# Kernel tuning notes

Hardware: AMD Instinct MI355X
Metric: run time of the kernel (lower is better)

Reference implementation:

```python
import jax, jax.numpy as jnp
import numpy as np
import itertools

# 3x3x3 neighborhood geometry: 27 cells, offsets in itertools.product order,
# so index 13 is the center voxel.
_POS = np.array(list(itertools.product([-1, 0, 1], repeat=3)))  # [27,3]
_DIFF = _POS[:, None, :] - _POS[None, :, :]
_A18 = (np.abs(_DIFF).sum(-1) <= 2)   # 18-connectivity (scipy structure s in source)
_A26 = (np.abs(_DIFF).max(-1) <= 1)   # 26-connectivity (np.ones((3,3,3)))
_CENTER = 13


def _cc_label_6(fg):
    """Connected-component labels of 3D bool array under 6-connectivity
    (scipy.ndimage.label default structure). Background = 0; each component
    gets a distinct positive id (min linear index + 1) via min-propagation."""
    n = fg.size
    BIG = jnp.int32(n + 2)
    idx = jnp.arange(1, n + 1, dtype=jnp.int32).reshape(fg.shape)
    lab0 = jnp.where(fg, idx, BIG)

    def step(lab):
        p = jnp.pad(lab, 1, mode='constant', constant_values=n + 2)
        m = lab
        m = jnp.minimum(m, p[:-2, 1:-1, 1:-1])
        m = jnp.minimum(m, p[2:, 1:-1, 1:-1])
        m = jnp.minimum(m, p[1:-1, :-2, 1:-1])
        m = jnp.minimum(m, p[1:-1, 2:, 1:-1])
        m = jnp.minimum(m, p[1:-1, 1:-1, :-2])
        m = jnp.minimum(m, p[1:-1, 1:-1, 2:])
        return jnp.where(fg, m, BIG)

    def cond(c):
        return c[1]

    def body(c):
        lab = c[0]
        new = step(lab)
        return (new, jnp.any(new != lab))

    lab, _ = jax.lax.while_loop(cond, body, (lab0, jnp.array(True)))
    return jnp.where(fg, lab, 0)


def _count_components(mask, adj_np):
    """mask: [V,27] bool. Counts connected components of the True cells in each
    27-cell neighborhood under adjacency adj_np (matches scipy label num_features).
    Min-label propagation for 26 steps (>= max path length in a 27-node graph)."""
    BIG = jnp.int32(27)
    ids = jnp.arange(27, dtype=jnp.int32)
    adj = jnp.asarray(adj_np)
    init = jnp.where(mask, ids[None, :], BIG)

    def body(_, lab):
        new = lab
        for j in range(27):
            contrib = jnp.where(mask[:, j], lab[:, j], BIG)[:, None]  # [V,1]
            new = jnp.minimum(new, jnp.where(adj[:, j][None, :], contrib, BIG))
        return jnp.where(mask, new, BIG)

    lab = jax.lax.fori_loop(0, 26, body, init)
    # a component's root keeps its own index -> count roots
    return jnp.sum(mask & (lab == ids[None, :]), axis=1)  # [V]


def _nonsimple_points(x, threshold=0.5):
    """JAX version of label_nonsimple_points: 1.0 where voxel is a non-simple
    point of the thresholded volume, else 0.0."""
    D, H, W = x.shape
    fg = x > threshold
    lab = _cc_label_6(fg)                       # [D,H,W] int32, 0 = background
    p = jnp.pad(lab, 1, mode='edge')            # np.pad(..., 'edge') in source
    nb = jnp.stack(
        [p[dz + 1:dz + 1 + D, dy + 1:dy + 1 + H, dx + 1:dx + 1 + W]
         for dz, dy, dx in _POS], axis=-1).reshape(-1, 27)  # [V,27]
    center = nb[:, _CENTER]
    # Test 1: cells differing from the center's component id (incl. background),
    # 18-connectivity; simple requires exactly one component.
    c1 = _count_components(nb != center[:, None], _A18)
    # Test 2: cells equal to the center's component, center removed,
    # 26-connectivity; simple requires exactly one component.
    m2 = (nb == center[:, None]).at[:, _CENTER].set(False)
    c2 = _count_components(m2, _A26)
    ns = (center != 0) & ((c1 != 1) | (c2 != 1))
    return ns.reshape(x.shape).astype(x.dtype)


def _weight_tensor(x, simple_weight=1.0, non_simple_weight=10.0):
    ns = jax.lax.stop_gradient(_nonsimple_points(x))
    w = simple_weight * (1.0 - ns) + non_simple_weight * ns
    return w * x


def setup_inputs() -> dict:
    key = jax.random.key(0)
    k1, k2 = jax.random.split(key)
    pred = jax.random.normal(k1, (64, 64, 64), dtype=jnp.float32)
    target = jax.random.uniform(k2, (64, 64, 64), dtype=jnp.float32)
    return {"pred": pred, "target": target}


def reference(pred, target):
    wp = _weight_tensor(pred)
    wl = _weight_tensor(target)
    # err = -(wl * -log(1+e^{-wp}) + (1-wl) * -log(1+e^{wp}))
    err = wl * jax.nn.softplus(-wp) + (1.0 - wl) * jax.nn.softplus(wp)
    return jnp.sum(err)
```

## Files before the change

### kernel.cpp

```cpp
#include <hip/hip_runtime.h>

#define NINV 0xFFFFFFFFu
static constexpr int D = 64, H = 64, W = 64;
static constexpr int NVOX = D * H * W;
static constexpr int NTOT = 2 * NVOX;


__device__ __forceinline__ unsigned find_c(unsigned* P, unsigned i) {
    unsigned p = P[i];
    while (p != i) {
        unsigned gp = P[p];
        if (gp == p) return p;
        P[i] = gp;
        i = gp;
        p = P[i];
    }
    return i;
}

__device__ void unite(unsigned* P, unsigned a, unsigned b) {
    for (;;) {
        a = find_c(P, a);
        b = find_c(P, b);
        if (a == b) return;
        if (a > b) { unsigned t = a; a = b; b = t; }
        unsigned old = atomicCAS(&P[b], b, a);
        if (old == b || old == a) return;
        b = old;
    }
}


__global__ __launch_bounds__(512) void local_ccl_k(const float* __restrict__ pred,
                                                   const float* __restrict__ target,
                                                   unsigned* __restrict__ parent) {
    __shared__ unsigned lab[512];
    int tb  = blockIdx.x & 511;
    int vol = blockIdx.x >> 9;
    const float* src = vol ? target : pred;
    int tx = (tb & 7) << 3;
    int ty = ((tb >> 3) & 7) << 3;
    int tz = (tb >> 6) << 3;

    int l = threadIdx.x;
    int lx = l & 7, ly = (l >> 3) & 7, lz = l >> 6;
    int g = ((tz + lz) << 12) + ((ty + ly) << 6) + (tx + lx);

    bool fg = src[g] > 0.5f;
    lab[l] = fg ? (unsigned)l : NINV;
    __syncthreads();

    for (;;) {
        int my_changed = 0;
        if (fg) {
            unsigned cur = lab[l];
            unsigned m = cur;
            if (lx > 0) m = min(m, lab[l - 1]);
            if (lx < 7) m = min(m, lab[l + 1]);
            if (ly > 0) m = min(m, lab[l - 8]);
            if (ly < 7) m = min(m, lab[l + 8]);
            if (lz > 0) m = min(m, lab[l - 64]);
            if (lz < 7) m = min(m, lab[l + 64]);
            for (;;) { unsigned p = lab[m]; if (p >= m) break; m = p; }
            if (m < cur) { lab[l] = m; my_changed = 1; }
        }
        if (__syncthreads_count(my_changed) == 0) break;
    }

    unsigned r = NINV;
    if (fg) {
        unsigned rr = lab[l];
        r = (unsigned)(vol * NVOX)
          + (unsigned)(((tz + (int)(rr >> 6)) << 12)
                     + ((ty + (int)((rr >> 3) & 7)) << 6)
                     +  (tx + (int)(rr & 7)));
    }
    parent[vol * NVOX + g] = r;
}


static constexpr int FACES_PER_DIR = 7 * 8 * 8;
static constexpr int FACES_PER_VOL = 3 * FACES_PER_DIR;
static constexpr int FACES_TOT     = 2 * FACES_PER_VOL;

__global__ void merge_k(unsigned* __restrict__ parent) {
    int wave = (int)((blockIdx.x * blockDim.x + threadIdx.x) >> 6);
    int lane = threadIdx.x & 63;
    if (wave >= FACES_TOT) return;
    int vol = wave / FACES_PER_VOL;
    int f   = wave - vol * FACES_PER_VOL;
    int dir = f / FACES_PER_DIR;
    int ff  = f - dir * FACES_PER_DIR;
    int plane = ff >> 6;
    int tf    = ff & 63;
    int a0 = ((tf & 7) << 3) + (lane & 7);
    int a1 = ((tf >> 3) << 3) + (lane >> 3);
    int x, y, z, stride;
    if (dir == 0)      { x = plane * 8 + 7; y = a0; z = a1; stride = 1; }
    else if (dir == 1) { y = plane * 8 + 7; x = a0; z = a1; stride = 64; }
    else               { z = plane * 8 + 7; x = a0; y = a1; stride = 4096; }
    int i = vol * NVOX + (z << 12) + (y << 6) + x;

    unsigned ra = parent[i];
    unsigned rb = parent[i + stride];
    bool valid = (ra != NINV) && (rb != NINV);
    unsigned long long key = valid ? (((unsigned long long)ra << 32) | rb) : ~0ull;

    bool leader = valid;
    #pragma unroll 8
    for (int j = 0; j < 64; ++j) {
        unsigned long long kj = __shfl(key, j, 64);
        if (j < lane && kj == key) leader = false;
    }
    if (leader) unite(parent, ra, rb);
}


__global__ void flatten_k(unsigned* __restrict__ parent) {
    int i = blockIdx.x * blockDim.x + threadIdx.x;
    if (i >= NTOT) return;
    unsigned p = parent[i];
    if (p == NINV) return;
    unsigned r = p, q;
    while ((q = parent[r]) != r) r = q;
    parent[i] = r;
}


__device__ __forceinline__ int count_components(unsigned mask, const unsigned* adj) {
    int count = 0;
    while (mask) {
        unsigned comp = mask & (0u - mask);
        for (;;) {
            unsigned acc = comp;
            unsigned t = comp;
            while (t) {
                int b = __ffs(t) - 1;
                acc |= adj[b];
                t &= t - 1;
            }
            acc &= mask;
            if (acc == comp) break;
            comp = acc;
        }
        mask &= ~comp;
        ++count;
    }
    return count;
}

__device__ __forceinline__ float weight_lds(const unsigned* __restrict__ h,
                                            int lx, int ly, int lz,
                                            const unsigned* sA18, const unsigned* sA26) {
    int ctr = (lz + 1) * 100 + (ly + 1) * 10 + (lx + 1);
    unsigned c = h[ctr];
    if (c == NINV) return 1.0f;
    unsigned same = 0;
    int k = 0;
    #pragma unroll
    for (int dz = 0; dz <= 2; ++dz) {
        #pragma unroll
        for (int dy = 0; dy <= 2; ++dy) {
            int base = (lz + dz) * 100 + (ly + dy) * 10 + lx;
            #pragma unroll
            for (int dx = 0; dx <= 2; ++dx) {
                same |= (h[base + dx] == c ? 1u : 0u) << k;
                ++k;
            }
        }
    }
    unsigned mask1 = (~same) & 0x07FFFFFFu;
    unsigned mask2 = same & ~(1u << 13);
    int c1 = count_components(mask1, sA18);
    int c2 = count_components(mask2, sA26);
    return ((c1 != 1) || (c2 != 1)) ? 10.0f : 1.0f;
}

__global__ __launch_bounds__(512) void final_k(const float* __restrict__ pred,
                                               const float* __restrict__ target,
                                               const unsigned* __restrict__ labP,
                                               const unsigned* __restrict__ labT,
                                               float* __restrict__ out) {
    __shared__ unsigned sA18[27], sA26[27];
    __shared__ unsigned hP[1000], hT[1000];
    __shared__ float sred[8];

    int l = threadIdx.x;
    if (l < 27) {
        int iz = l / 9, iy = (l / 3) % 3, ix = l % 3;
        unsigned m18 = 0, m26 = 0;
        for (int j = 0; j < 27; ++j) {
            int jz = j / 9, jy = (j / 3) % 3, jx = j % 3;
            int az = iz - jz; az = az < 0 ? -az : az;
            int ay = iy - jy; ay = ay < 0 ? -ay : ay;
            int ax = ix - jx; ax = ax < 0 ? -ax : ax;
            if (az + ay + ax <= 2) m18 |= 1u << j;
            if (az <= 1 && ay <= 1 && ax <= 1) m26 |= 1u << j;
        }
        sA18[l] = m18; sA26[l] = m26;
    }

    int tb = blockIdx.x;
    int tx = (tb & 7) << 3;
    int ty = ((tb >> 3) & 7) << 3;
    int tz = (tb >> 6) << 3;

    for (int e = l; e < 1000; e += 512) {
        int hx = e % 10, hy = (e / 10) % 10, hz = e / 100;
        int gx = min(max(tx + hx - 1, 0), 63);
        int gy = min(max(ty + hy - 1, 0), 63);
        int gz = min(max(tz + hz - 1, 0), 63);
        int g = (gz << 12) + (gy << 6) + gx;
        hP[e] = labP[g];
        hT[e] = labT[g];
    }
    __syncthreads();

    int lx = l & 7, ly = (l >> 3) & 7, lz = l >> 6;
    int g = ((tz + lz) << 12) + ((ty + ly) << 6) + (tx + lx);

    float wP = weight_lds(hP, lx, ly, lz, sA18, sA26);
    float wT = weight_lds(hT, lx, ly, lz, sA18, sA26);
    float wp = wP * pred[g];
    float wl = wT * target[g];
    float l1pe = log1pf(expf(-fabsf(wp)));
    float sp_pos = fmaxf(wp, 0.0f) + l1pe;
    float sp_neg = fmaxf(-wp, 0.0f) + l1pe;
    float err = wl * sp_neg + (1.0f - wl) * sp_pos;

    #pragma unroll
    for (int o = 32; o > 0; o >>= 1) err += __shfl_down(err, o, 64);
    int lane = l & 63;
    int wv = l >> 6;
    if (lane == 0) sred[wv] = err;
    __syncthreads();
    if (l == 0) {
        float s = 0.0f;
        #pragma unroll
        for (int w = 0; w < 8; ++w) s += sred[w];
        atomicAdd(out, s);
    }
}


extern "C" void kernel_launch(void* const* d_in, const int* in_sizes, int n_in,
                              void* d_out, int out_size, void* d_ws, size_t ws_size,
                              hipStream_t stream) {
    const float* pred   = (const float*)d_in[0];
    const float* target = (const float*)d_in[1];
    float* out = (float*)d_out;
    unsigned* parent = (unsigned*)d_ws;

    hipMemsetAsync(d_out, 0, sizeof(float), stream);

    local_ccl_k<<<1024, 512, 0, stream>>>(pred, target, parent);
    merge_k<<<FACES_TOT * 64 / 256, 256, 0, stream>>>(parent);
    flatten_k<<<NTOT / 256, 256, 0, stream>>>(parent);
    final_k<<<512, 512, 0, stream>>>(pred, target, parent, parent + NVOX, out);
}
```

Before: 124.6 us.

## Use bit-parallel dilation for component tests and fold flatten into final kernel

```diff
diff --git a/kernel.cpp b/kernel.cpp
--- a/kernel.cpp
+++ b/kernel.cpp
@@ -116,42 +116,60 @@
 }
 
 
-__global__ void flatten_k(unsigned* __restrict__ parent) {
-    int i = blockIdx.x * blockDim.x + threadIdx.x;
-    if (i >= NTOT) return;
-    unsigned p = parent[i];
-    if (p == NINV) return;
-    unsigned r = p, q;
-    while ((q = parent[r]) != r) r = q;
-    parent[i] = r;
-}
-
-
-__device__ __forceinline__ int count_components(unsigned mask, const unsigned* adj) {
-    int count = 0;
-    while (mask) {
-        unsigned comp = mask & (0u - mask);
-        for (;;) {
-            unsigned acc = comp;
-            unsigned t = comp;
-            while (t) {
-                int b = __ffs(t) - 1;
-                acc |= adj[b];
-                t &= t - 1;
-            }
-            acc &= mask;
-            if (acc == comp) break;
-            comp = acc;
-        }
-        mask &= ~comp;
-        ++count;
-    }
-    return count;
+static constexpr unsigned ALL27 = 0x7FFFFFFu;
+static constexpr unsigned XL2 = 0x36DB6DBu;
+static constexpr unsigned XG0 = 0x6DB6DB6u;
+static constexpr unsigned YL2 = 0x0FC7E3Fu;
+static constexpr unsigned YG0 = 0x7E3F1F8u;
+static constexpr unsigned ZL2 = 0x003FFFFu;
+static constexpr unsigned ZG0 = 0x7FFFE00u;
+static constexpr unsigned X0  = 0x1249249u;
+static constexpr unsigned X2  = 0x4924924u;
+static constexpr unsigned Y0  = 0x01C0E07u;
+static constexpr unsigned Y2  = 0x70381C0u;
+static constexpr unsigned Z0  = 0x00001FFu;
+static constexpr unsigned Z2  = 0x7FC0000u;
+
+__device__ __forceinline__ unsigned dilX(unsigned m) {
+    return m | ((m & XL2) << 1) | ((m & XG0) >> 1);
+}
+__device__ __forceinline__ unsigned dilY(unsigned m) {
+    return m | ((m & YL2) << 3) | ((m & YG0) >> 3);
+}
+__device__ __forceinline__ unsigned dilZ(unsigned m) {
+    return m | ((m & ZL2) << 9) | ((m & ZG0) >> 9);
+}
+__device__ __forceinline__ unsigned dil2(unsigned m) {
+    return ((m & X0) << 2) | ((m & X2) >> 2)
+         | ((m & Y0) << 6) | ((m & Y2) >> 6)
+         | ((m & Z0) << 18) | ((m & Z2) >> 18);
+}
+
+__device__ __forceinline__ bool multi18(unsigned mask) {
+    if (mask == 0) return true;
+    unsigned comp = mask & (0u - mask);
+    for (;;) {
+        unsigned a = dilX(comp), b = dilY(comp);
+        unsigned n = (dilY(a) | dilZ(a) | dilZ(b) | dil2(comp)) & mask;
+        if (n == comp) break;
+        comp = n;
+    }
+    return comp != mask;
+}
+
+__device__ __forceinline__ bool multi26(unsigned mask) {
+    if (mask == 0) return true;
+    unsigned comp = mask & (0u - mask);
+    for (;;) {
+        unsigned n = dilZ(dilY(dilX(comp))) & mask;
+        if (n == comp) break;
+        comp = n;
+    }
+    return comp != mask;
 }
 
 __device__ __forceinline__ float weight_lds(const unsigned* __restrict__ h,
-                                            int lx, int ly, int lz,
-                                            const unsigned* sA18, const unsigned* sA26) {
+                                            int lx, int ly, int lz) {
     int ctr = (lz + 1) * 100 + (ly + 1) * 10 + (lx + 1);
     unsigned c = h[ctr];
     if (c == NINV) return 1.0f;
@@ -169,37 +187,20 @@
             }
         }
     }
-    unsigned mask1 = (~same) & 0x07FFFFFFu;
-    unsigned mask2 = same & ~(1u << 13);
-    int c1 = count_components(mask1, sA18);
-    int c2 = count_components(mask2, sA26);
-    return ((c1 != 1) || (c2 != 1)) ? 10.0f : 1.0f;
+    unsigned m1 = (~same) & ALL27;
+    unsigned m2 = same & ~(1u << 13);
+    bool ns = multi18(m1) || multi26(m2);
+    return ns ? 10.0f : 1.0f;
 }
 
 __global__ __launch_bounds__(512) void final_k(const float* __restrict__ pred,
                                                const float* __restrict__ target,
-                                               const unsigned* __restrict__ labP,
-                                               const unsigned* __restrict__ labT,
+                                               unsigned* __restrict__ parent,
                                                float* __restrict__ out) {
-    __shared__ unsigned sA18[27], sA26[27];
     __shared__ unsigned hP[1000], hT[1000];
     __shared__ float sred[8];
 
     int l = threadIdx.x;
-    if (l < 27) {
-        int iz = l / 9, iy = (l / 3) % 3, ix = l % 3;
-        unsigned m18 = 0, m26 = 0;
-        for (int j = 0; j < 27; ++j) {
-            int jz = j / 9, jy = (j / 3) % 3, jx = j % 3;
-            int az = iz - jz; az = az < 0 ? -az : az;
-            int ay = iy - jy; ay = ay < 0 ? -ay : ay;
-            int ax = ix - jx; ax = ax < 0 ? -ax : ax;
-            if (az + ay + ax <= 2) m18 |= 1u << j;
-            if (az <= 1 && ay <= 1 && ax <= 1) m26 |= 1u << j;
-        }
-        sA18[l] = m18; sA26[l] = m26;
-    }
-
     int tb = blockIdx.x;
     int tx = (tb & 7) << 3;
     int ty = ((tb >> 3) & 7) << 3;
@@ -211,16 +212,20 @@
         int gy = min(max(ty + hy - 1, 0), 63);
         int gz = min(max(tz + hz - 1, 0), 63);
         int g = (gz << 12) + (gy << 6) + gx;
-        hP[e] = labP[g];
-        hT[e] = labT[g];
+        unsigned p = parent[g];
+        if (p != NINV) { unsigned q; while ((q = parent[p]) != p) p = q; }
+        hP[e] = p;
+        unsigned s = parent[NVOX + g];
+        if (s != NINV) { unsigned q; while ((q = parent[s]) != s) s = q; }
+        hT[e] = s;
     }
     __syncthreads();
 
     int lx = l & 7, ly = (l >> 3) & 7, lz = l >> 6;
     int g = ((tz + lz) << 12) + ((ty + ly) << 6) + (tx + lx);
 
-    float wP = weight_lds(hP, lx, ly, lz, sA18, sA26);
-    float wT = weight_lds(hT, lx, ly, lz, sA18, sA26);
+    float wP = weight_lds(hP, lx, ly, lz);
+    float wT = weight_lds(hT, lx, ly, lz);
     float wp = wP * pred[g];
     float wl = wT * target[g];
     float l1pe = log1pf(expf(-fabsf(wp)));
@@ -255,6 +260,5 @@
 
     local_ccl_k<<<1024, 512, 0, stream>>>(pred, target, parent);
     merge_k<<<FACES_TOT * 64 / 256, 256, 0, stream>>>(parent);
-    flatten_k<<<NTOT / 256, 256, 0, stream>>>(parent);
-    final_k<<<512, 512, 0, stream>>>(pred, target, parent, parent + NVOX, out);
-}
+    final_k<<<512, 512, 0, stream>>>(pred, target, parent, out);
+}
```

Measured after the change: 111.0 us. 1.12x faster.
